# Kernel tuning notes

Hardware: AMD Instinct MI355X
Metric: run time of the kernel (lower is better)

The kernel has to match this reference:

```python
import math
import jax, jax.numpy as jnp
import numpy as np

H = 16  # head_count
D = 1024  # model_dim
DH = D // H  # dim_per_head = 64
PAD_IDX = 1


def setup_inputs() -> dict:
    key = jax.random.key(0)
    ks = jax.random.split(key, 16)
    B, L = 4, 512
    s = 0.02
    inp = {
        'key': jax.random.normal(ks[0], (B, L, D), jnp.float32),
        'value': jax.random.normal(ks[1], (B, L, D), jnp.float32),
        'query': jax.random.normal(ks[2], (B, L, D), jnp.float32),
        'ast_parents_matrix': jax.random.randint(ks[3], (B, L, L), 0, 200, jnp.int32),
        'mask': jnp.zeros((B, 1, L), jnp.bool_),
        'Wq': jax.random.normal(ks[4], (D, D), jnp.float32) * s,
        'bq': jnp.zeros((D,), jnp.float32),
        'Wk': jax.random.normal(ks[5], (D, D), jnp.float32) * s,
        'bk': jnp.zeros((D,), jnp.float32),
        'Wv': jax.random.normal(ks[6], (D, D), jnp.float32) * s,
        'bv': jnp.zeros((D,), jnp.float32),
        'Wo': jax.random.normal(ks[7], (D, D), jnp.float32) * s,
        'bo': jnp.zeros((D,), jnp.float32),
        'struct_emb': jax.random.normal(ks[8], (200, DH), jnp.float32).at[PAD_IDX].set(0.0),
        'value_emb': jax.random.normal(ks[9], (10000, DH), jnp.float32).at[PAD_IDX].set(0.0),
    }
    return inp


def _parent_embeddings(matrix, struct_emb, value_emb):
    # matrix: (B, Lq, K) int ids; even key positions use structure vocab, odd use value vocab
    B, Lq, K = matrix.shape
    s_ids = matrix[:, :, ::2]   # (B, Lq, ceil(K/2))
    v_ids = matrix[:, :, 1::2]  # (B, Lq, floor(K/2))
    emb_s = struct_emb[s_ids]   # (B, Lq, S, DH)
    emb_v = value_emb[v_ids]    # (B, Lq, V, DH)
    S = emb_s.shape[2]
    if emb_v.shape[2] != S:  # odd K: pad value stream by one zero slot, drop after interleave
        emb_v = jnp.concatenate([emb_v, jnp.zeros_like(emb_s[:, :, :1])], axis=2)
    pe = jnp.stack([emb_s, emb_v], axis=3).reshape(B, Lq, 2 * S, DH)
    return pe[:, :, :K, :]  # (B, Lq, K, DH)


def reference(key, value, query, ast_parents_matrix, mask,
              Wq, bq, Wk, bk, Wv, bv, Wo, bo, struct_emb, value_emb):
    B, L, _ = query.shape

    def shape(x):
        return x.reshape(B, -1, H, DH).transpose(0, 2, 1, 3)  # (B,H,L,DH)

    q = shape(query @ Wq + bq) / math.sqrt(DH)
    k = shape(key @ Wk + bk)
    v = shape(value @ Wv + bv)

    qk = jnp.einsum('bhid,bhjd->bhij', q, k)  # (B,H,L,L)

    pe = _parent_embeddings(ast_parents_matrix[:, :, :L], struct_emb, value_emb)
    score_ast = jnp.einsum('bhid,bijd->bhij', q, pe)

    scores = (qk + score_ast).astype(jnp.float32)
    scores = jnp.where(mask[:, None, :, :], -1e18, scores)  # mask: (B,1,L)->(B,1,1,L)
    attn = jax.nn.softmax(scores, axis=-1).astype(q.dtype)
    # dropout p=0.0 (eval) -> identity
    context = jnp.einsum('bhij,bhjd->bhid', attn, v)  # (B,H,L,DH)
    context = context.transpose(0, 2, 1, 3).reshape(B, L, D)
    output = context @ Wo + bo
    return output, attn
```

## Files before the change

kernel.cpp:

```cpp
#include <hip/hip_runtime.h>
#include <cstddef>

#define H 16
#define D 1024
#define DH 64
#define L 512

typedef __attribute__((ext_vector_type(8))) short bf16x8;
typedef __attribute__((ext_vector_type(4))) short bf16x4;
typedef __attribute__((ext_vector_type(4))) float f32x4;
typedef __attribute__((ext_vector_type(4))) unsigned u32x4;
typedef __attribute__((ext_vector_type(2))) unsigned u32x2;

__device__ inline short f2bf(float x) {
    union { float f; unsigned u; } c; c.f = x;
    unsigned r = (c.u + 0x7FFFu + ((c.u >> 16) & 1u)) >> 16;
    return (short)r;
}
__device__ inline float bf2f(short x) {
    union { float f; unsigned u; } c;
    c.u = ((unsigned)(unsigned short)x) << 16; return c.f;
}

__device__ inline void gload_lds16(const void* g, void* l) {
    __builtin_amdgcn_global_load_lds(
        (const __attribute__((address_space(1))) unsigned int*)g,
        (__attribute__((address_space(3))) unsigned int*)l,
        16, 0, 0);
}

__device__ inline bf16x8 agl16(const short* p) {
    u32x4 r;
    asm volatile("global_load_dwordx4 %0, %1, off" : "=&v"(r) : "v"(p) : "memory");
    union { u32x4 u; bf16x8 v; } c; c.u = r; return c.v;
}
__device__ inline bf16x4 agl8(const short* p) {
    u32x2 r;
    asm volatile("global_load_dwordx2 %0, %1, off" : "=&v"(r) : "v"(p) : "memory");
    union { u32x2 u; bf16x4 v; } c; c.u = r; return c.v;
}
__device__ inline unsigned agl4(const void* p) {
    unsigned r;
    asm volatile("global_load_dword %0, %1, off" : "=&v"(r) : "v"(p) : "memory");
    return r;
}
__device__ inline void wait_vm0_fence() {
    asm volatile("s_waitcnt vmcnt(0)" ::: "memory");
    __builtin_amdgcn_sched_barrier(0);
}

struct PrepArgs {
    const float* csrc[5]; short* cdst[5]; int cn[5];
    const float* W[4]; short* T[4];
};

__global__ __launch_bounds__(256) void prep_kernel(PrepArgs a) {
    const int y = blockIdx.y;
    if (y < 5) {
        const float* s = a.csrc[y];
        short* d = a.cdst[y];
        int n = a.cn[y];
        int i = (blockIdx.x * 256 + threadIdx.x) * 8;
        if (i >= n) return;
        float4 x0 = *(const float4*)(s + i);
        float4 x1 = *(const float4*)(s + i + 4);
        bf16x8 o;
        o[0] = f2bf(x0.x); o[1] = f2bf(x0.y); o[2] = f2bf(x0.z); o[3] = f2bf(x0.w);
        o[4] = f2bf(x1.x); o[5] = f2bf(x1.y); o[6] = f2bf(x1.z); o[7] = f2bf(x1.w);
        *(bf16x8*)(d + i) = o;
    } else {
        const float* W = a.W[y - 5];
        short* T = a.T[y - 5];
        int idx = blockIdx.x * 256 + threadIdx.x;
        if (idx >= 1024 * 128) return;
        int n = idx & 1023;
        int k0 = (idx >> 10) << 3;
        bf16x8 o;
        #pragma unroll
        for (int kk = 0; kk < 8; ++kk)
            o[kk] = f2bf(W[(size_t)(k0 + kk) * 1024 + n]);
        *(bf16x8*)(T + (size_t)n * 1024 + k0) = o;
    }
}

#define BM 128
#define BN 64
#define BKK 64

struct GemmBatch {
    const short* A[3]; const short* Bt[3]; const float* bias[3];
    void* out[3]; float scale[3]; int mode[3];
};

__global__ __launch_bounds__(256) void gemm_mfma_kernel(GemmBatch P, int M, int N, int K) {
    const int z = blockIdx.z;
    const short* __restrict__ A  = P.A[z];
    const short* __restrict__ Bt = P.Bt[z];
    const float* __restrict__ bias = P.bias[z];
    const float scale = P.scale[z];
    const int mode = P.mode[z];

    __shared__ short lds[(BM + BN) * BKK];
    short* As = lds;
    short* Bs = lds + BM * BKK;

    const int tid = threadIdx.x;
    const int wave = tid >> 6, lane = tid & 63;
    const int fm = lane & 15, quad = lane >> 4;
    const int m0 = blockIdx.y * BM, n0 = blockIdx.x * BN;

    int arow[4], acol[4];
    #pragma unroll
    for (int t = 0; t < 4; ++t) {
        int s = (wave * 4 + t) * 64 + lane;
        int row = s >> 3;
        int u = (s & 7) ^ (row & 7);
        arow[t] = row; acol[t] = u * 8;
    }
    int brow[2], bcol[2];
    #pragma unroll
    for (int t = 0; t < 2; ++t) {
        int s = (wave * 2 + t) * 64 + lane;
        int row = s >> 3;
        int u = (s & 7) ^ (row & 7);
        brow[t] = row; bcol[t] = u * 8;
    }

    int aoff[2][2], boff[4][2];
    #pragma unroll
    for (int mt = 0; mt < 2; ++mt)
        #pragma unroll
        for (int kst = 0; kst < 2; ++kst) {
            int row = wave * 32 + mt * 16 + fm;
            int u = quad + 4 * kst;
            aoff[mt][kst] = row * 64 + ((u ^ (row & 7)) * 8);
        }
    #pragma unroll
    for (int nt = 0; nt < 4; ++nt)
        #pragma unroll
        for (int kst = 0; kst < 2; ++kst) {
            int row = nt * 16 + fm;
            int u = quad + 4 * kst;
            boff[nt][kst] = row * 64 + ((u ^ (row & 7)) * 8);
        }

    f32x4 acc[2][4];
    #pragma unroll
    for (int mt = 0; mt < 2; ++mt)
        #pragma unroll
        for (int nt = 0; nt < 4; ++nt) acc[mt][nt] = (f32x4){0.f, 0.f, 0.f, 0.f};

    for (int k0 = 0; k0 < K; k0 += BKK) {
        __syncthreads();
        #pragma unroll
        for (int t = 0; t < 4; ++t)
            gload_lds16(A + (size_t)(m0 + arow[t]) * K + k0 + acol[t],
                        As + (wave * 4 + t) * 512);
        #pragma unroll
        for (int t = 0; t < 2; ++t)
            gload_lds16(Bt + (size_t)(n0 + brow[t]) * K + k0 + bcol[t],
                        Bs + (wave * 2 + t) * 512);
        __syncthreads();
        #pragma unroll
        for (int kst = 0; kst < 2; ++kst) {
            bf16x8 af[2], bfr[4];
            af[0] = *(const bf16x8*)(As + aoff[0][kst]);
            af[1] = *(const bf16x8*)(As + aoff[1][kst]);
            #pragma unroll
            for (int nt = 0; nt < 4; ++nt)
                bfr[nt] = *(const bf16x8*)(Bs + boff[nt][kst]);
            #pragma unroll
            for (int mt = 0; mt < 2; ++mt)
                #pragma unroll
                for (int nt = 0; nt < 4; ++nt)
                    acc[mt][nt] = __builtin_amdgcn_mfma_f32_16x16x32_bf16(
                        af[mt], bfr[nt], acc[mt][nt], 0, 0, 0);
        }
    }

    if (mode == 2) {
        __syncthreads();
        short (*T)[BM + 8] = (short(*)[BM + 8])&lds[0];
        #pragma unroll
        for (int mt = 0; mt < 2; ++mt)
            #pragma unroll
            for (int nt = 0; nt < 4; ++nt) {
                int nn = nt * 16 + fm;
                float bv = bias[n0 + nn];
                #pragma unroll
                for (int r = 0; r < 4; ++r) {
                    int mm = wave * 32 + mt * 16 + quad * 4 + r;
                    T[nn][mm] = f2bf((acc[mt][nt][r] + bv) * scale);
                }
            }
        __syncthreads();
        int b = m0 >> 9;
        int ibase = m0 & (L - 1);
        int hblk = n0 >> 6;
        int n = tid >> 2, seg = (tid & 3) * 32;
        short* dst = (short*)P.out[z] + (((size_t)(b * H + hblk) * DH + n) * L) + ibase + seg;
        #pragma unroll
        for (int c = 0; c < 4; ++c)
            *(bf16x8*)(dst + c * 8) = *(const bf16x8*)(&T[n][seg + c * 8]);
    } else {
        #pragma unroll
        for (int mt = 0; mt < 2; ++mt)
            #pragma unroll
            for (int nt = 0; nt < 4; ++nt) {
                int n = n0 + nt * 16 + fm;
                float bv = bias[n];
                #pragma unroll
                for (int r = 0; r < 4; ++r) {
                    int m = m0 + wave * 32 + mt * 16 + quad * 4 + r;
                    float val = (acc[mt][nt][r] + bv) * scale;
                    if (mode == 0) {
                        ((float*)P.out[z])[(size_t)m * N + n] = val;
                    } else {
                        int b = m >> 9, i = m & (L - 1);
                        int h = n >> 6, d = n & (DH - 1);
                        ((short*)P.out[z])[(((size_t)(b * H + h) * L + i) * DH) + d] = f2bf(val);
                    }
                }
            }
    }
}

__global__ __launch_bounds__(256) void ast_kernel(
    const short* __restrict__ Qb, const int* __restrict__ mat,
    const short* __restrict__ semb, const short* __restrict__ vemb,
    short* __restrict__ Sast)
{
    const int i = blockIdx.x, b = blockIdx.y;
    const int tid = threadIdx.x;
    const int wave = tid >> 6, lane = tid & 63;
    const int fm = lane & 15, quad = lane >> 4;
    __shared__ short Sl[H][L + 8];

    const short* qp = Qb + (((size_t)(b * H + fm) * L + i) * DH);
    bf16x8 a0 = *(const bf16x8*)(qp + quad * 8);
    bf16x8 a1 = *(const bf16x8*)(qp + 32 + quad * 8);

    const int* mrow = mat + ((size_t)b * L + i) * L;

    int idxs[8];
    const short* ebase[8];
    #pragma unroll
    for (int t = 0; t < 8; ++t) {
        int j = (wave + t * 4) * 16 + fm;
        idxs[t] = mrow[j];
    }
    #pragma unroll
    for (int t = 0; t < 8; ++t) {
        int j = (wave + t * 4) * 16 + fm;
        ebase[t] = ((j & 1) ? vemb : semb) + (size_t)idxs[t] * DH;
    }

    #pragma unroll
    for (int t = 0; t < 8; ++t) {
        int j = (wave + t * 4) * 16 + fm;
        bf16x8 b0 = *(const bf16x8*)(ebase[t] + quad * 8);
        bf16x8 b1 = *(const bf16x8*)(ebase[t] + 32 + quad * 8);
        f32x4 c = {0.f, 0.f, 0.f, 0.f};
        c = __builtin_amdgcn_mfma_f32_16x16x32_bf16(a0, b0, c, 0, 0, 0);
        c = __builtin_amdgcn_mfma_f32_16x16x32_bf16(a1, b1, c, 0, 0, 0);
        #pragma unroll
        for (int r = 0; r < 4; ++r)
            Sl[quad * 4 + r][j] = f2bf(c[r]);
    }
    __syncthreads();
    int hh = tid >> 4, j0 = (tid & 15) * 32;
    short* dst = Sast + ((((size_t)b * L + i) * H + hh) * L) + j0;
    #pragma unroll
    for (int c = 0; c < 4; ++c)
        *(bf16x8*)(dst + c * 8) = *(const bf16x8*)(&Sl[hh][j0 + c * 8]);
}

__global__ __launch_bounds__(256, 3) void attn_fused_kernel(
    const short* __restrict__ Qb, const short* __restrict__ Kb,
    const short* __restrict__ Vt, const short* __restrict__ Sast,
    const unsigned char* __restrict__ mask,
    float* __restrict__ attn, short* __restrict__ ctx)
{
    const int flat = blockIdx.x + (blockIdx.y << 5) + (blockIdx.z << 9);
    const int xcd = flat & 7;
    const int slot = flat >> 3;
    const int pair = ((slot >> 5) << 3) + xcd;
    const int i0 = (slot & 31) * 16;
    const int h = pair & 15;
    const int b = pair >> 4;

    const int tid = threadIdx.x;
    const int wave = tid >> 6, lane = tid & 63;
    const int fm = lane & 15, quad = lane >> 4;
    const int jw = wave * 128;

    __shared__ short Pl[16][520];
    __shared__ float red_m[4][16];
    __shared__ float red_l[4][16];

    const short* qp = Qb + (((size_t)(b * H + h) * L + i0 + fm) * DH);
    bf16x8 q0 = *(const bf16x8*)(qp + quad * 8);
    bf16x8 q1 = *(const bf16x8*)(qp + 32 + quad * 8);
    const short* Kbase = Kb + ((size_t)(b * H + h) * L) * DH;
    const short* sastrow = Sast + (((size_t)b * L + i0 + fm) * H + h) * L;
    const unsigned char* mrow = mask + (size_t)b * L + jw;

    bf16x8 kf0[8], kf1[8];
    bf16x4 sa[8];
    unsigned mku[8];
    #pragma unroll
    for (int t = 0; t < 8; ++t) {
        const short* kr = Kbase + (size_t)(jw + t * 16 + fm) * DH;
        kf0[t] = agl16(kr + quad * 8);
        kf1[t] = agl16(kr + 32 + quad * 8);
        sa[t]  = agl8(sastrow + jw + t * 16 + quad * 4);
        mku[t] = agl4(mrow + t * 16 + quad * 4);
    }
    wait_vm0_fence();

    float s[8][4];
    float mx = -3.0e38f;
    #pragma unroll
    for (int t = 0; t < 8; ++t) {
        f32x4 c = {0.f, 0.f, 0.f, 0.f};
        c = __builtin_amdgcn_mfma_f32_16x16x32_bf16(kf0[t], q0, c, 0, 0, 0);
        c = __builtin_amdgcn_mfma_f32_16x16x32_bf16(kf1[t], q1, c, 0, 0, 0);
        #pragma unroll
        for (int r = 0; r < 4; ++r) {
            float sv = c[r] + bf2f(sa[t][r]);
            sv = ((mku[t] >> (8 * r)) & 255u) ? -1e18f : sv;
            s[t][r] = sv;
            mx = fmaxf(mx, sv);
        }
    }

    bf16x8 vf[16];
    const short* Vb = Vt + (((size_t)(b * H + h) * DH + wave * 16 + fm) * L);
    #pragma unroll
    for (int i = 0; i < 16; ++i)
        vf[i] = agl16(Vb + i * 32 + quad * 8);

    mx = fmaxf(mx, __shfl_xor(mx, 16));
    mx = fmaxf(mx, __shfl_xor(mx, 32));

    float sum = 0.f;
    #pragma unroll
    for (int t = 0; t < 8; ++t)
        #pragma unroll
        for (int r = 0; r < 4; ++r) {
            float e = __expf(s[t][r] - mx);
            s[t][r] = e;
            sum += e;
        }
    sum += __shfl_xor(sum, 16);
    sum += __shfl_xor(sum, 32);
    if (quad == 0) {
        red_m[wave][fm] = mx;
        red_l[wave][fm] = sum;
    }
    __syncthreads();

    float m0_ = red_m[0][fm], m1_ = red_m[1][fm];
    float m2_ = red_m[2][fm], m3_ = red_m[3][fm];
    float M_ = fmaxf(fmaxf(m0_, m1_), fmaxf(m2_, m3_));
    float T_ = red_l[0][fm] * __expf(m0_ - M_)
             + red_l[1][fm] * __expf(m1_ - M_)
             + red_l[2][fm] * __expf(m2_ - M_)
             + red_l[3][fm] * __expf(m3_ - M_);
    float fac = __expf(mx - M_) / T_;

    float* arow = attn + (((size_t)(b * H + h) * L + i0 + fm) * L);
    #pragma unroll
    for (int t = 0; t < 8; ++t) {
        int jt = jw + t * 16 + quad * 4;
        bf16x4 pw;
        #pragma unroll
        for (int r = 0; r < 4; ++r)
            pw[r] = f2bf(s[t][r] * fac);
        *(bf16x4*)(&Pl[fm][jt]) = pw;
        float4 v;
        v.x = bf2f(pw[0]); v.y = bf2f(pw[1]); v.z = bf2f(pw[2]); v.w = bf2f(pw[3]);
        *(float4*)(arow + jt) = v;
    }
    __syncthreads();

    wait_vm0_fence();
    f32x4 o = {0.f, 0.f, 0.f, 0.f};
    #pragma unroll
    for (int ks = 0; ks < 16; ++ks) {
        bf16x8 pa = *(const bf16x8*)(&Pl[fm][ks * 32 + quad * 8]);
        o = __builtin_amdgcn_mfma_f32_16x16x32_bf16(pa, vf[ks], o, 0, 0, 0);
    }
    #pragma unroll
    for (int r = 0; r < 4; ++r)
        ctx[((size_t)b * L + i0 + quad * 4 + r) * D + h * DH + wave * 16 + fm] = f2bf(o[r]);
}

extern "C" void kernel_launch(void* const* d_in, const int* in_sizes, int n_in,
                              void* d_out, int out_size, void* d_ws, size_t ws_size,
                              hipStream_t stream) {
    const float* key_in   = (const float*)d_in[0];
    const float* value_in = (const float*)d_in[1];
    const float* query_in = (const float*)d_in[2];
    const int*   mat      = (const int*)d_in[3];
    const unsigned char* mask = (const unsigned char*)d_in[4];
    const float* Wq = (const float*)d_in[5];
    const float* bq = (const float*)d_in[6];
    const float* Wk = (const float*)d_in[7];
    const float* bk = (const float*)d_in[8];
    const float* Wv = (const float*)d_in[9];
    const float* bv = (const float*)d_in[10];
    const float* Wo = (const float*)d_in[11];
    const float* bo = (const float*)d_in[12];
    const float* struct_emb = (const float*)d_in[13];
    const float* value_emb  = (const float*)d_in[14];

    const int B = in_sizes[2] / (L * D);
    const int M = B * L;

    short* p = (short*)d_ws;
    short* xk  = p;  p += (size_t)M * D;
    short* xv  = p;  p += (size_t)M * D;
    short* xq  = p;  p += (size_t)M * D;
    short* WqT = p;  p += (size_t)D * D;
    short* WkT = p;  p += (size_t)D * D;
    short* WvT = p;  p += (size_t)D * D;
    short* WoT = p;  p += (size_t)D * D;
    short* semb = p; p += 16384;
    short* vemb = p; p += (size_t)in_sizes[14];
    short* Qb = p;   p += (size_t)M * D;
    short* Kb = p;   p += (size_t)M * D;
    short* Vt = p;   p += (size_t)M * D;
    short* Sast = p; p += (size_t)B * L * H * L;
    short* ctx = xk;

    float* out_p  = (float*)d_out;
    float* attn_p = out_p + (size_t)M * D;

    PrepArgs pa;
    pa.csrc[0] = key_in;     pa.cdst[0] = xk;   pa.cn[0] = M * D;
    pa.csrc[1] = value_in;   pa.cdst[1] = xv;   pa.cn[1] = M * D;
    pa.csrc[2] = query_in;   pa.cdst[2] = xq;   pa.cn[2] = M * D;
    pa.csrc[3] = struct_emb; pa.cdst[3] = semb; pa.cn[3] = in_sizes[13];
    pa.csrc[4] = value_emb;  pa.cdst[4] = vemb; pa.cn[4] = in_sizes[14];
    pa.W[0] = Wq; pa.W[1] = Wk; pa.W[2] = Wv; pa.W[3] = Wo;
    pa.T[0] = WqT; pa.T[1] = WkT; pa.T[2] = WvT; pa.T[3] = WoT;
    prep_kernel<<<dim3((M * D) / 2048, 9), 256, 0, stream>>>(pa);

    GemmBatch qkv;
    qkv.A[0] = xq; qkv.Bt[0] = WqT; qkv.bias[0] = bq; qkv.out[0] = Qb; qkv.scale[0] = 0.125f; qkv.mode[0] = 1;
    qkv.A[1] = xk; qkv.Bt[1] = WkT; qkv.bias[1] = bk; qkv.out[1] = Kb; qkv.scale[1] = 1.0f;   qkv.mode[1] = 1;
    qkv.A[2] = xv; qkv.Bt[2] = WvT; qkv.bias[2] = bv; qkv.out[2] = Vt; qkv.scale[2] = 1.0f;   qkv.mode[2] = 2;
    gemm_mfma_kernel<<<dim3(D / BN, M / BM, 3), 256, 0, stream>>>(qkv, M, D, D);

    ast_kernel<<<dim3(L, B), 256, 0, stream>>>(Qb, mat, semb, vemb, Sast);

    attn_fused_kernel<<<dim3(L / 16, H, B), 256, 0, stream>>>(
        Qb, Kb, Vt, Sast, mask, attn_p, ctx);

    GemmBatch fin;
    fin.A[0] = ctx; fin.Bt[0] = WoT; fin.bias[0] = bo; fin.out[0] = out_p; fin.scale[0] = 1.0f; fin.mode[0] = 0;
    fin.A[1] = ctx; fin.Bt[1] = WoT; fin.bias[1] = bo; fin.out[1] = out_p; fin.scale[1] = 1.0f; fin.mode[1] = 0;
    fin.A[2] = ctx; fin.Bt[2] = WoT; fin.bias[2] = bo; fin.out[2] = out_p; fin.scale[2] = 1.0f; fin.mode[2] = 0;
    gemm_mfma_kernel<<<dim3(D / BN, M / BM, 1), 256, 0, stream>>>(fin, M, D, D);
}
```

Baseline: 240.4 us.

## Split Q projection and co-schedule K/V GEMM with AST score kernel

The Q projection now runs as its own GEMM launch. The K and V projections are merged into one launch with the AST structural score computation, with blockIdx.y selecting between GEMM tiles and AST rows. Because the AST work only needs Q, it can fill the GPU alongside the K/V GEMM instead of running as a separate serialized launch, which removes tail idle time and one launch. The cost is an extra Q-only launch, shared-memory sizing set by the larger user, and heterogeneous blocks inside one grid.

```diff
diff --git a/kernel.cpp b/kernel.cpp
--- a/kernel.cpp
+++ b/kernel.cpp
@@ -92,22 +92,17 @@
     void* out[3]; float scale[3]; int mode[3];
 };
 
-__global__ __launch_bounds__(256) void gemm_mfma_kernel(GemmBatch P, int M, int N, int K) {
-    const int z = blockIdx.z;
-    const short* __restrict__ A  = P.A[z];
-    const short* __restrict__ Bt = P.Bt[z];
-    const float* __restrict__ bias = P.bias[z];
-    const float scale = P.scale[z];
-    const int mode = P.mode[z];
-
-    __shared__ short lds[(BM + BN) * BKK];
+__device__ __forceinline__ void gemm_tile_body(
+    const short* __restrict__ A, const short* __restrict__ Bt,
+    const float* __restrict__ bias, void* out, float scale, int mode,
+    int M, int N, int K, int bx, int by, short* lds, int tid)
+{
     short* As = lds;
     short* Bs = lds + BM * BKK;
 
-    const int tid = threadIdx.x;
     const int wave = tid >> 6, lane = tid & 63;
     const int fm = lane & 15, quad = lane >> 4;
-    const int m0 = blockIdx.y * BM, n0 = blockIdx.x * BN;
+    const int m0 = by * BM, n0 = bx * BN;
 
     int arow[4], acol[4];
     #pragma unroll
@@ -198,7 +193,7 @@
         int ibase = m0 & (L - 1);
         int hblk = n0 >> 6;
         int n = tid >> 2, seg = (tid & 3) * 32;
-        short* dst = (short*)P.out[z] + (((size_t)(b * H + hblk) * DH + n) * L) + ibase + seg;
+        short* dst = (short*)out + (((size_t)(b * H + hblk) * DH + n) * L) + ibase + seg;
         #pragma unroll
         for (int c = 0; c < 4; ++c)
             *(bf16x8*)(dst + c * 8) = *(const bf16x8*)(&T[n][seg + c * 8]);
@@ -214,27 +209,32 @@
                     int m = m0 + wave * 32 + mt * 16 + quad * 4 + r;
                     float val = (acc[mt][nt][r] + bv) * scale;
                     if (mode == 0) {
-                        ((float*)P.out[z])[(size_t)m * N + n] = val;
+                        ((float*)out)[(size_t)m * N + n] = val;
                     } else {
                         int b = m >> 9, i = m & (L - 1);
                         int h = n >> 6, d = n & (DH - 1);
-                        ((short*)P.out[z])[(((size_t)(b * H + h) * L + i) * DH) + d] = f2bf(val);
+                        ((short*)out)[(((size_t)(b * H + h) * L + i) * DH) + d] = f2bf(val);
                     }
                 }
             }
     }
 }
 
-__global__ __launch_bounds__(256) void ast_kernel(
+__global__ __launch_bounds__(256) void gemm_mfma_kernel(GemmBatch P, int M, int N, int K) {
+    __shared__ short lds[(BM + BN) * BKK];
+    const int z = blockIdx.z;
+    gemm_tile_body(P.A[z], P.Bt[z], P.bias[z], P.out[z], P.scale[z], P.mode[z],
+                   M, N, K, blockIdx.x, blockIdx.y, lds, threadIdx.x);
+}
+
+__device__ __forceinline__ void ast_body(
     const short* __restrict__ Qb, const int* __restrict__ mat,
     const short* __restrict__ semb, const short* __restrict__ vemb,
-    short* __restrict__ Sast)
+    short* __restrict__ Sast, int i, int b, int tid, short* shmem)
 {
-    const int i = blockIdx.x, b = blockIdx.y;
-    const int tid = threadIdx.x;
     const int wave = tid >> 6, lane = tid & 63;
     const int fm = lane & 15, quad = lane >> 4;
-    __shared__ short Sl[H][L + 8];
+    short (*Sl)[L + 8] = (short(*)[L + 8])shmem;
 
     const short* qp = Qb + (((size_t)(b * H + fm) * L + i) * DH);
     bf16x8 a0 = *(const bf16x8*)(qp + quad * 8);
@@ -273,6 +273,26 @@
     #pragma unroll
     for (int c = 0; c < 4; ++c)
         *(bf16x8*)(dst + c * 8) = *(const bf16x8*)(&Sl[hh][j0 + c * 8]);
+}
+
+__global__ __launch_bounds__(256) void kv_ast_kernel(
+    GemmBatch P, int M, int N, int K,
+    const short* __restrict__ Qb, const int* __restrict__ mat,
+    const short* __restrict__ semb, const short* __restrict__ vemb,
+    short* __restrict__ Sast)
+{
+    __shared__ short shmem[(BM + BN) * BKK];
+    if (blockIdx.y == 0) {
+        int x = blockIdx.x;
+        int z = x >> 8;
+        int rem = x & 255;
+        int by = rem >> 4, bx = rem & 15;
+        gemm_tile_body(P.A[z], P.Bt[z], P.bias[z], P.out[z], P.scale[z], P.mode[z],
+                       M, N, K, bx, by, shmem, threadIdx.x);
+    } else {
+        ast_body(Qb, mat, semb, vemb, Sast, blockIdx.x, blockIdx.y - 1,
+                 threadIdx.x, shmem);
+    }
 }
 
 __global__ __launch_bounds__(256, 3) void attn_fused_kernel(
@@ -447,20 +467,20 @@
     pa.T[0] = WqT; pa.T[1] = WkT; pa.T[2] = WvT; pa.T[3] = WoT;
     prep_kernel<<<dim3((M * D) / 2048, 9), 256, 0, stream>>>(pa);
 
-    GemmBatch qkv;
-    qkv.A[0] = xq; qkv.Bt[0] = WqT; qkv.bias[0] = bq; qkv.out[0] = Qb; qkv.scale[0] = 0.125f; qkv.mode[0] = 1;
-    qkv.A[1] = xk; qkv.Bt[1] = WkT; qkv.bias[1] = bk; qkv.out[1] = Kb; qkv.scale[1] = 1.0f;   qkv.mode[1] = 1;
-    qkv.A[2] = xv; qkv.Bt[2] = WvT; qkv.bias[2] = bv; qkv.out[2] = Vt; qkv.scale[2] = 1.0f;   qkv.mode[2] = 2;
-    gemm_mfma_kernel<<<dim3(D / BN, M / BM, 3), 256, 0, stream>>>(qkv, M, D, D);
-
-    ast_kernel<<<dim3(L, B), 256, 0, stream>>>(Qb, mat, semb, vemb, Sast);
+    GemmBatch qonly;
+    qonly.A[0] = xq; qonly.Bt[0] = WqT; qonly.bias[0] = bq; qonly.out[0] = Qb;
+    qonly.scale[0] = 0.125f; qonly.mode[0] = 1;
+    gemm_mfma_kernel<<<dim3(D / BN, M / BM, 1), 256, 0, stream>>>(qonly, M, D, D);
+
+    GemmBatch kv;
+    kv.A[0] = xk; kv.Bt[0] = WkT; kv.bias[0] = bk; kv.out[0] = Kb; kv.scale[0] = 1.0f; kv.mode[0] = 1;
+    kv.A[1] = xv; kv.Bt[1] = WvT; kv.bias[1] = bv; kv.out[1] = Vt; kv.scale[1] = 1.0f; kv.mode[1] = 2;
+    kv_ast_kernel<<<dim3(512, 5), 256, 0, stream>>>(kv, M, D, D, Qb, mat, semb, vemb, Sast);
 
     attn_fused_kernel<<<dim3(L / 16, H, B), 256, 0, stream>>>(
         Qb, Kb, Vt, Sast, mask, attn_p, ctx);
 
     GemmBatch fin;
     fin.A[0] = ctx; fin.Bt[0] = WoT; fin.bias[0] = bo; fin.out[0] = out_p; fin.scale[0] = 1.0f; fin.mode[0] = 0;
-    fin.A[1] = ctx; fin.Bt[1] = WoT; fin.bias[1] = bo; fin.out[1] = out_p; fin.scale[1] = 1.0f; fin.mode[1] = 0;
-    fin.A[2] = ctx; fin.Bt[2] = WoT; fin.bias[2] = bo; fin.out[2] = out_p; fin.scale[2] = 1.0f; fin.mode[2] = 0;
     gemm_mfma_kernel<<<dim3(D / BN, M / BM, 1), 256, 0, stream>>>(fin, M, D, D);
 }
```

Result: slower. 249.2 us (+3.6%).
